# Kernel optimization log

Measured on AMD Instinct MI355X. Metric: run time of the kernel, lower is better.

The kernel has to match this reference:

```python
import jax, jax.numpy as jnp
import numpy as np

N_NODES = 100000
N_EDGES = 3200000
F_IN = 256
N_CLASSES = 10


def setup_inputs() -> dict:
    key = jax.random.key(0)
    ks = jax.random.split(key, 10)
    x = jax.random.normal(ks[0], (N_NODES, F_IN), dtype=jnp.float32)
    edge_index = jax.random.randint(ks[1], (2, N_EDGES), 0, N_NODES, dtype=jnp.int64)
    def glorot(k, fan_in, fan_out):
        s = (6.0 / (fan_in + fan_out)) ** 0.5
        return jax.random.uniform(k, (fan_in, fan_out), jnp.float32, -s, s)
    return {
        "x": x,
        "edge_index": edge_index,
        "W_gcn": glorot(ks[2], F_IN, 64),
        "b_gcn": jnp.zeros((64,), jnp.float32),
        "W1": glorot(ks[3], 64, 32),
        "b1": jnp.zeros((32,), jnp.float32),
        "W2": glorot(ks[4], 32, 16),
        "b2": jnp.zeros((16,), jnp.float32),
        "W3": glorot(ks[5], 16, N_CLASSES),
        "b3": jnp.zeros((N_CLASSES,), jnp.float32),
    }


def gcn_conv(x, edge_index, W, b):
    # PyG GCNConv: x' = D^{-1/2} (A + I) D^{-1/2} (x W) + b, with self-loops.
    n = x.shape[0]
    loop = jnp.arange(n, dtype=edge_index.dtype)
    src = jnp.concatenate([edge_index[0], loop])  # [E+N]
    dst = jnp.concatenate([edge_index[1], loop])
    deg = jax.ops.segment_sum(jnp.ones(src.shape, jnp.float32), dst, num_segments=n)
    dinv = jnp.where(deg > 0, jax.lax.rsqrt(deg), 0.0)
    norm = dinv[src] * dinv[dst]  # [E+N]
    h = x @ W  # transform first (reduces message width to 64)
    msg = h[src] * norm[:, None]  # gather + scale
    out = jax.ops.segment_sum(msg, dst, num_segments=n)  # scatter-add
    return out + b


def reference(x, edge_index, W_gcn, b_gcn, W1, b1, W2, b2, W3, b3):
    # Dropout is a no-op in eval mode; reference uses deterministic eval math.
    h = jax.nn.relu(gcn_conv(x, edge_index, W_gcn, b_gcn))
    h = jax.nn.relu(h @ W1 + b1)
    h = jax.nn.relu(h @ W2 + b2)
    return h @ W3 + b3
```

## Files before the change

### kernel.cpp

```cpp
#include <hip/hip_runtime.h>

#define F_IN 256
#define CHUNK 8192
#define PMAX 24

typedef short bf8_t __attribute__((ext_vector_type(8)));
typedef float f4_t  __attribute__((ext_vector_type(4)));

__device__ __forceinline__ unsigned short f2bf(float f) {
  unsigned u = __float_as_uint(f);
  unsigned r = (u + 0x7FFFu + ((u >> 16) & 1u)) >> 16;
  return (unsigned short)r;
}
#define BF_LO(d) __uint_as_float((d) << 16)
#define BF_HI(d) __uint_as_float((d) & 0xFFFF0000u)

__global__ __launch_bounds__(256) void gemm_mfma_kernel(
    const float* __restrict__ x, const float* __restrict__ W,
    const float* __restrict__ dinvp, unsigned short* __restrict__ hb, int M) {
  __shared__ short As[128][40];
  __shared__ short Bs[64][264];
  const int t = threadIdx.x;
  const int brow = blockIdx.x * 128;
  const int w = t >> 6;
  const int l = t & 63;
  const int mlane = l & 15;
  const int quad = l >> 4;

  for (int i = 0; i < 64; ++i) {
    const int flat = i * 256 + t;
    const int k = flat >> 6, n = flat & 63;
    Bs[n][k] = (short)f2bf(W[flat]);
  }

  f4_t acc[2][4];
#pragma unroll
  for (int a = 0; a < 2; ++a)
#pragma unroll
    for (int b = 0; b < 4; ++b) acc[a][b] = (f4_t){0.f, 0.f, 0.f, 0.f};

  for (int k0 = 0; k0 < F_IN; k0 += 32) {
    {
      const int q = t & 7;
      const int rbase = t >> 3;
#pragma unroll
      for (int j = 0; j < 4; ++j) {
        const int r = rbase + j * 32;
        const int row = brow + r;
        float4 v = make_float4(0.f, 0.f, 0.f, 0.f);
        if (row < M) v = *(const float4*)(x + (size_t)row * F_IN + k0 + (q << 2));
        short* p = &As[r][q << 2];
        p[0] = (short)f2bf(v.x);
        p[1] = (short)f2bf(v.y);
        p[2] = (short)f2bf(v.z);
        p[3] = (short)f2bf(v.w);
      }
    }
    __syncthreads();
    bf8_t afr[2], bfr[4];
#pragma unroll
    for (int mt = 0; mt < 2; ++mt)
      afr[mt] = *(const bf8_t*)&As[w * 32 + mt * 16 + mlane][quad << 3];
#pragma unroll
    for (int nt = 0; nt < 4; ++nt)
      bfr[nt] = *(const bf8_t*)&Bs[nt * 16 + mlane][k0 + (quad << 3)];
#pragma unroll
    for (int mt = 0; mt < 2; ++mt)
#pragma unroll
      for (int nt = 0; nt < 4; ++nt)
        acc[mt][nt] = __builtin_amdgcn_mfma_f32_16x16x32_bf16(
            afr[mt], bfr[nt], acc[mt][nt], 0, 0, 0);
    __syncthreads();
  }

#pragma unroll
  for (int mt = 0; mt < 2; ++mt) {
#pragma unroll
    for (int reg = 0; reg < 4; ++reg) {
      const int row = brow + w * 32 + mt * 16 + (quad << 2) + reg;
      if (row < M) {
        const float di = dinvp[row];
#pragma unroll
        for (int nt = 0; nt < 4; ++nt)
          hb[(size_t)row * 64 + nt * 16 + mlane] = f2bf(di * acc[mt][nt][reg]);
      }
    }
  }
}

__global__ __launch_bounds__(512) void sort_local_kernel(
    const int* __restrict__ src_arr, const int* __restrict__ dst_arr,
    int* __restrict__ espB, int* __restrict__ segStart, int* __restrict__ segCnt,
    int* __restrict__ bucketCount, int E, int NBK) {
  __shared__ int hist[512];
  __shared__ int s[512];
  __shared__ int cur[512];
  const int t = threadIdx.x;
  const int blk = blockIdx.x;
  const int base = blk * CHUNK;
  const int cnt = min(CHUNK, E - base);
  for (int i = t; i < NBK; i += 512) hist[i] = 0;
  __syncthreads();
  int pk[16], bk[16];
#pragma unroll
  for (int k = 0; k < 16; ++k) {
    const int i = t + k * 512;
    bk[k] = -1;
    if (i < cnt) {
      const int sv = src_arr[base + i];
      const int dv = dst_arr[base + i];
      pk[k] = sv | ((dv & 255) << 24);
      bk[k] = dv >> 8;
      atomicAdd(&hist[bk[k]], 1);
    }
  }
  __syncthreads();
  const int v = (t < NBK) ? hist[t] : 0;
  s[t] = v;
  __syncthreads();
#pragma unroll
  for (int off = 1; off < 512; off <<= 1) {
    int add = (t >= off) ? s[t - off] : 0;
    __syncthreads();
    s[t] += add;
    __syncthreads();
  }
  if (t < NBK) {
    const int excl = s[t] - v;
    cur[t] = excl;
    segStart[blk * NBK + t] = base + excl;
    segCnt[blk * NBK + t] = v;
    if (v) atomicAdd(&bucketCount[t], v);
  }
  __syncthreads();
#pragma unroll
  for (int k = 0; k < 16; ++k) {
    if (bk[k] >= 0) {
      const int pos = atomicAdd(&cur[bk[k]], 1);
      espB[base + pos] = pk[k];
    }
  }
}

__global__ __launch_bounds__(512) void scan_buckets_kernel(
    const int* __restrict__ bucketCount, int* __restrict__ bucketStart, int NBK) {
  __shared__ int s[512];
  const int t = threadIdx.x;
  const int v = (t < NBK) ? bucketCount[t] : 0;
  s[t] = v;
  __syncthreads();
#pragma unroll
  for (int off = 1; off < 512; off <<= 1) {
    int add = (t >= off) ? s[t - off] : 0;
    __syncthreads();
    s[t] += add;
    __syncthreads();
  }
  if (t < NBK) bucketStart[t] = s[t] - v;
  if (t == NBK - 1) bucketStart[NBK] = s[t];
}

__global__ __launch_bounds__(512) void fine_bin2_kernel(
    const int* __restrict__ espB, const int* __restrict__ segStart,
    const int* __restrict__ segCnt, const int* __restrict__ bucketStart,
    int* __restrict__ es, int* __restrict__ rowptr, float* __restrict__ dinvp,
    int N, int E, int NBK, int NCH) {
  __shared__ int segO[513];
  __shared__ int segS[512];
  __shared__ int s[512];
  __shared__ int hist[256];
  __shared__ int cur[256];
  const int t = threadIdx.x;
  const int b = blockIdx.x;
  int c = 0;
  if (t < NCH) {
    segS[t] = segStart[t * NBK + b];
    c = segCnt[t * NBK + b];
  }
  s[t] = c;
  if (t < 256) hist[t] = 0;
  __syncthreads();
#pragma unroll
  for (int off = 1; off < 512; off <<= 1) {
    int add = (t >= off) ? s[t - off] : 0;
    __syncthreads();
    s[t] += add;
    __syncthreads();
  }
  segO[t + 1] = s[t];
  if (t == 0) segO[0] = 0;
  __syncthreads();
  const int total = segO[NCH];
  const int base = bucketStart[b];

  int pc[PMAX];
  int it = 0;
  for (int j = t; j < total; j += 512, ++it) {
    int lo = 0, hi = NCH;
    while (hi - lo > 1) {
      const int mid = (lo + hi) >> 1;
      if (segO[mid] <= j) lo = mid; else hi = mid;
    }
    const int p = espB[segS[lo] + (j - segO[lo])];
    if (it < PMAX) pc[it] = p;
    atomicAdd(&hist[((unsigned)p) >> 24], 1);
  }
  __syncthreads();
  const int v2 = (t < 256) ? hist[t] : 0;
  s[t] = v2;
  __syncthreads();
#pragma unroll
  for (int off = 1; off < 256; off <<= 1) {
    int add = (t >= off) ? s[t - off] : 0;
    __syncthreads();
    s[t] += add;
    __syncthreads();
  }
  if (t < 256) {
    const int excl = s[t] - v2;
    cur[t] = base + excl;
    const int node = b * 256 + t;
    if (node < N) {
      rowptr[node] = base + excl;
      dinvp[node] = rsqrtf((float)(v2 + 1));
    }
  }
  if (b == 0 && t == 0) rowptr[N] = E;
  __syncthreads();
  it = 0;
  for (int j = t; j < total; j += 512, ++it) {
    int p;
    if (it < PMAX) {
      p = pc[it];
    } else {
      int lo = 0, hi = NCH;
      while (hi - lo > 1) {
        const int mid = (lo + hi) >> 1;
        if (segO[mid] <= j) lo = mid; else hi = mid;
      }
      p = espB[segS[lo] + (j - segO[lo])];
    }
    const int pos = atomicAdd(&cur[((unsigned)p) >> 24], 1);
    es[pos] = p & 0x00FFFFFF;
  }
}

__global__ __launch_bounds__(256) void agg_csr_kernel(
    const unsigned short* __restrict__ hb, const int* __restrict__ es,
    const int* __restrict__ rowptr, const float* __restrict__ dinvp,
    float* __restrict__ agg, int N) {
  const int t = threadIdx.x;
  const int node = blockIdx.x * 4 + (t >> 6);
  if (node >= N) return;
  const int lane = t & 63;
  const int slot = lane >> 3;
  const int fq = (lane & 7) << 3;
  const int start = rowptr[node];
  const int end = rowptr[node + 1];

  float acc[8] = {0.f};
  int i = start + slot;
  for (; i + 8 < end; i += 16) {
    const int s0 = es[i];
    const int s1 = es[i + 8];
    const uint4 r0 = *(const uint4*)(hb + (size_t)s0 * 64 + fq);
    const uint4 r1 = *(const uint4*)(hb + (size_t)s1 * 64 + fq);
    acc[0] += BF_LO(r0.x) + BF_LO(r1.x);
    acc[1] += BF_HI(r0.x) + BF_HI(r1.x);
    acc[2] += BF_LO(r0.y) + BF_LO(r1.y);
    acc[3] += BF_HI(r0.y) + BF_HI(r1.y);
    acc[4] += BF_LO(r0.z) + BF_LO(r1.z);
    acc[5] += BF_HI(r0.z) + BF_HI(r1.z);
    acc[6] += BF_LO(r0.w) + BF_LO(r1.w);
    acc[7] += BF_HI(r0.w) + BF_HI(r1.w);
  }
  if (i < end) {
    const int s0 = es[i];
    const uint4 r0 = *(const uint4*)(hb + (size_t)s0 * 64 + fq);
    acc[0] += BF_LO(r0.x);
    acc[1] += BF_HI(r0.x);
    acc[2] += BF_LO(r0.y);
    acc[3] += BF_HI(r0.y);
    acc[4] += BF_LO(r0.z);
    acc[5] += BF_HI(r0.z);
    acc[6] += BF_LO(r0.w);
    acc[7] += BF_HI(r0.w);
  }
#pragma unroll
  for (int m = 8; m <= 32; m <<= 1)
#pragma unroll
    for (int j = 0; j < 8; ++j) acc[j] += __shfl_xor(acc[j], m, 64);

  if (slot == 0) {
    const float di = dinvp[node];
    float4 o0 = make_float4(acc[0] * di, acc[1] * di, acc[2] * di, acc[3] * di);
    float4 o1 = make_float4(acc[4] * di, acc[5] * di, acc[6] * di, acc[7] * di);
    float* ap = agg + (size_t)node * 64 + fq;
    *(float4*)(ap + 0) = o0;
    *(float4*)(ap + 4) = o1;
  }
}

__global__ __launch_bounds__(256) void mlp_kernel(
    const float* __restrict__ agg, const unsigned short* __restrict__ hb,
    const float* __restrict__ dinvp, const float* __restrict__ bg,
    const float* __restrict__ W1, const float* __restrict__ b1,
    const float* __restrict__ W2, const float* __restrict__ b2,
    const float* __restrict__ W3, const float* __restrict__ b3,
    float* __restrict__ out, int N) {
  __shared__ float W1T[32][64];
  __shared__ float W2T[16][32];
  __shared__ float W3T[10][16];
  __shared__ float b1s[32], b2s[16], b3s[10], bgs[64];
  const int t = threadIdx.x;
  for (int i = t; i < 2048; i += 256) W1T[i >> 6][i & 63] = W1[(i & 63) * 32 + (i >> 6)];
  for (int i = t; i < 512; i += 256)  W2T[i >> 5][i & 31] = W2[(i & 31) * 16 + (i >> 5)];
  for (int i = t; i < 160; i += 256)  W3T[i >> 4][i & 15] = W3[(i & 15) * 10 + (i >> 4)];
  if (t < 64) bgs[t] = bg[t];
  if (t < 32) b1s[t] = b1[t];
  if (t < 16) b2s[t] = b2[t];
  if (t < 10) b3s[t] = b3[t];
  __syncthreads();

  const int node = blockIdx.x * 256 + t;
  if (node >= N) return;
  const float di = dinvp[node];

  float g[64];
#pragma unroll
  for (int k = 0; k < 64; k += 8) {
    const float4 a0 = *(const float4*)(agg + (size_t)node * 64 + k);
    const float4 a1 = *(const float4*)(agg + (size_t)node * 64 + k + 4);
    const uint4 r = *(const uint4*)(hb + (size_t)node * 64 + k);
    g[k + 0] = fmaxf(a0.x + di * BF_LO(r.x) + bgs[k + 0], 0.f);
    g[k + 1] = fmaxf(a0.y + di * BF_HI(r.x) + bgs[k + 1], 0.f);
    g[k + 2] = fmaxf(a0.z + di * BF_LO(r.y) + bgs[k + 2], 0.f);
    g[k + 3] = fmaxf(a0.w + di * BF_HI(r.y) + bgs[k + 3], 0.f);
    g[k + 4] = fmaxf(a1.x + di * BF_LO(r.z) + bgs[k + 4], 0.f);
    g[k + 5] = fmaxf(a1.y + di * BF_HI(r.z) + bgs[k + 5], 0.f);
    g[k + 6] = fmaxf(a1.z + di * BF_LO(r.w) + bgs[k + 6], 0.f);
    g[k + 7] = fmaxf(a1.w + di * BF_HI(r.w) + bgs[k + 7], 0.f);
  }

  float h1[32];
#pragma unroll
  for (int j = 0; j < 32; ++j) {
    float acc = b1s[j];
#pragma unroll
    for (int k = 0; k < 64; k += 4) {
      const float4 w = *(const float4*)&W1T[j][k];
      acc += g[k] * w.x + g[k + 1] * w.y + g[k + 2] * w.z + g[k + 3] * w.w;
    }
    h1[j] = fmaxf(acc, 0.f);
  }

  float h2[16];
#pragma unroll
  for (int j = 0; j < 16; ++j) {
    float acc = b2s[j];
#pragma unroll
    for (int k = 0; k < 32; k += 4) {
      const float4 w = *(const float4*)&W2T[j][k];
      acc += h1[k] * w.x + h1[k + 1] * w.y + h1[k + 2] * w.z + h1[k + 3] * w.w;
    }
    h2[j] = fmaxf(acc, 0.f);
  }

#pragma unroll
  for (int j = 0; j < 10; ++j) {
    float acc = b3s[j];
#pragma unroll
    for (int k = 0; k < 16; k += 4) {
      const float4 w = *(const float4*)&W3T[j][k];
      acc += h2[k] * w.x + h2[k + 1] * w.y + h2[k + 2] * w.z + h2[k + 3] * w.w;
    }
    out[(size_t)node * 10 + j] = acc;
  }
}

extern "C" void kernel_launch(void* const* d_in, const int* in_sizes, int n_in,
                              void* d_out, int out_size, void* d_ws, size_t ws_size,
                              hipStream_t stream) {
  const float* x     = (const float*)d_in[0];
  const int*   ei    = (const int*)d_in[1];
  const float* W_gcn = (const float*)d_in[2];
  const float* b_gcn = (const float*)d_in[3];
  const float* W1    = (const float*)d_in[4];
  const float* b1    = (const float*)d_in[5];
  const float* W2    = (const float*)d_in[6];
  const float* b2    = (const float*)d_in[7];
  const float* W3    = (const float*)d_in[8];
  const float* b3    = (const float*)d_in[9];
  float* out = (float*)d_out;

  const int N = in_sizes[0] / F_IN;
  const int E = in_sizes[1] / 2;
  const int* src = ei;
  const int* dst = ei + E;
  const int NBK = (N + 255) >> 8;
  const int NCH = (E + CHUNK - 1) / CHUNK;

  unsigned short* hb = (unsigned short*)d_ws;
  float* dinvp       = (float*)(hb + (size_t)N * 64);
  int*   es          = (int*)(dinvp + N);
  int*   rowptr      = es + E;
  int*   bucketCount = rowptr + N + 16;
  int*   bucketStart = bucketCount + 512;
  int*   espB        = bucketStart + 528;
  int*   segStart    = espB + E;
  int*   segCnt      = segStart + NCH * NBK;
  float* agg         = (float*)espB;

  hipMemsetAsync(bucketCount, 0, 512 * sizeof(int), stream);

  sort_local_kernel<<<NCH, 512, 0, stream>>>(
      src, dst, espB, segStart, segCnt, bucketCount, E, NBK);
  scan_buckets_kernel<<<1, 512, 0, stream>>>(bucketCount, bucketStart, NBK);
  fine_bin2_kernel<<<NBK, 512, 0, stream>>>(
      espB, segStart, segCnt, bucketStart, es, rowptr, dinvp, N, E, NBK, NCH);

  gemm_mfma_kernel<<<(N + 127) / 128, 256, 0, stream>>>(x, W_gcn, dinvp, hb, N);

  agg_csr_kernel<<<(N + 3) / 4, 256, 0, stream>>>(hb, es, rowptr, dinvp, agg, N);

  mlp_kernel<<<(N + 255) / 256, 256, 0, stream>>>(
      agg, hb, dinvp, b_gcn, W1, b1, W2, b2, W3, b3, out, N);
}
```

Baseline: 367.9 us.

## Use MFMA bf16 for MLP head and simplify fine binning traversal

The per-node scalar FP32 MLP (64→32→16→10) is replaced by a block-tiled version that stages activations and weights in shared memory as bf16 and computes each layer with 16x16x32 bf16 MFMA instructions. The fine binning kernel drops its prefix scan over segments and the per-element binary search, and instead has each wavefront walk segments directly for both the histogram and scatter passes. This trades FP32 precision in the MLP for matrix-core throughput, and it removes register caching of edge values, so espB is read twice.

```diff
diff --git a/kernel.cpp b/kernel.cpp
--- a/kernel.cpp
+++ b/kernel.cpp
@@ -2,7 +2,6 @@
 
 #define F_IN 256
 #define CHUNK 8192
-#define PMAX 24
 
 typedef short bf8_t __attribute__((ext_vector_type(8)));
 typedef float f4_t  __attribute__((ext_vector_type(4)));
@@ -165,59 +164,46 @@
     const int* __restrict__ segCnt, const int* __restrict__ bucketStart,
     int* __restrict__ es, int* __restrict__ rowptr, float* __restrict__ dinvp,
     int N, int E, int NBK, int NCH) {
-  __shared__ int segO[513];
   __shared__ int segS[512];
-  __shared__ int s[512];
+  __shared__ int segC[512];
+  __shared__ int sbuf[512];
   __shared__ int hist[256];
   __shared__ int cur[256];
   const int t = threadIdx.x;
   const int b = blockIdx.x;
-  int c = 0;
-  if (t < NCH) {
-    segS[t] = segStart[t * NBK + b];
-    c = segCnt[t * NBK + b];
-  }
-  s[t] = c;
+  for (int i = t; i < 512; i += 512) { segS[i] = 0; segC[i] = 0; }
   if (t < 256) hist[t] = 0;
   __syncthreads();
-#pragma unroll
-  for (int off = 1; off < 512; off <<= 1) {
-    int add = (t >= off) ? s[t - off] : 0;
-    __syncthreads();
-    s[t] += add;
-    __syncthreads();
-  }
-  segO[t + 1] = s[t];
-  if (t == 0) segO[0] = 0;
-  __syncthreads();
-  const int total = segO[NCH];
+  for (int i = t; i < NCH; i += 512) {
+    segS[i] = segStart[i * NBK + b];
+    segC[i] = segCnt[i * NBK + b];
+  }
+  __syncthreads();
+
+  const int wid = t >> 6;
+  const int lane = t & 63;
+
+  for (int seg = wid; seg < NCH; seg += 8) {
+    const int sS = segS[seg], c = segC[seg];
+    for (int j = lane; j < c; j += 64)
+      atomicAdd(&hist[((unsigned)espB[sS + j]) >> 24], 1);
+  }
+  __syncthreads();
+
+  int v2 = 0;
+  if (t < 256) { v2 = hist[t]; sbuf[t] = v2; }
+  __syncthreads();
+#pragma unroll
+  for (int off = 1; off < 256; off <<= 1) {
+    int add = 0;
+    if (t < 256 && t >= off) add = sbuf[t - off];
+    __syncthreads();
+    if (t < 256) sbuf[t] += add;
+    __syncthreads();
+  }
   const int base = bucketStart[b];
-
-  int pc[PMAX];
-  int it = 0;
-  for (int j = t; j < total; j += 512, ++it) {
-    int lo = 0, hi = NCH;
-    while (hi - lo > 1) {
-      const int mid = (lo + hi) >> 1;
-      if (segO[mid] <= j) lo = mid; else hi = mid;
-    }
-    const int p = espB[segS[lo] + (j - segO[lo])];
-    if (it < PMAX) pc[it] = p;
-    atomicAdd(&hist[((unsigned)p) >> 24], 1);
-  }
-  __syncthreads();
-  const int v2 = (t < 256) ? hist[t] : 0;
-  s[t] = v2;
-  __syncthreads();
-#pragma unroll
-  for (int off = 1; off < 256; off <<= 1) {
-    int add = (t >= off) ? s[t - off] : 0;
-    __syncthreads();
-    s[t] += add;
-    __syncthreads();
-  }
   if (t < 256) {
-    const int excl = s[t] - v2;
+    const int excl = sbuf[t] - v2;
     cur[t] = base + excl;
     const int node = b * 256 + t;
     if (node < N) {
@@ -227,21 +213,14 @@
   }
   if (b == 0 && t == 0) rowptr[N] = E;
   __syncthreads();
-  it = 0;
-  for (int j = t; j < total; j += 512, ++it) {
-    int p;
-    if (it < PMAX) {
-      p = pc[it];
-    } else {
-      int lo = 0, hi = NCH;
-      while (hi - lo > 1) {
-        const int mid = (lo + hi) >> 1;
-        if (segO[mid] <= j) lo = mid; else hi = mid;
-      }
-      p = espB[segS[lo] + (j - segO[lo])];
-    }
-    const int pos = atomicAdd(&cur[((unsigned)p) >> 24], 1);
-    es[pos] = p & 0x00FFFFFF;
+
+  for (int seg = wid; seg < NCH; seg += 8) {
+    const int sS = segS[seg], c = segC[seg];
+    for (int j = lane; j < c; j += 64) {
+      const int p = espB[sS + j];
+      const int pos = atomicAdd(&cur[((unsigned)p) >> 24], 1);
+      es[pos] = p & 0x00FFFFFF;
+    }
   }
 }
 
@@ -301,80 +280,132 @@
   }
 }
 
-__global__ __launch_bounds__(256) void mlp_kernel(
+__global__ __launch_bounds__(256) void mlp_mfma_kernel(
     const float* __restrict__ agg, const unsigned short* __restrict__ hb,
     const float* __restrict__ dinvp, const float* __restrict__ bg,
     const float* __restrict__ W1, const float* __restrict__ b1,
     const float* __restrict__ W2, const float* __restrict__ b2,
     const float* __restrict__ W3, const float* __restrict__ b3,
     float* __restrict__ out, int N) {
-  __shared__ float W1T[32][64];
-  __shared__ float W2T[16][32];
-  __shared__ float W3T[10][16];
-  __shared__ float b1s[32], b2s[16], b3s[10], bgs[64];
-  const int t = threadIdx.x;
-  for (int i = t; i < 2048; i += 256) W1T[i >> 6][i & 63] = W1[(i & 63) * 32 + (i >> 6)];
-  for (int i = t; i < 512; i += 256)  W2T[i >> 5][i & 31] = W2[(i & 31) * 16 + (i >> 5)];
-  for (int i = t; i < 160; i += 256)  W3T[i >> 4][i & 15] = W3[(i & 15) * 10 + (i >> 4)];
+  __shared__ short g64[256 * 72];
+  __shared__ short h2s[256 * 40];
+  __shared__ short W1s[32 * 72];
+  __shared__ short W2s[16 * 40];
+  __shared__ short W3s[16 * 40];
+  __shared__ float bgs[64], b1s[32], b2s[16], b3s[16];
+  short* h1s = g64;
+
+  const int t = threadIdx.x;
+  const int node0 = blockIdx.x * 256;
+  for (int i = t; i < 256 * 40; i += 256) h2s[i] = 0;
+  for (int i = t; i < 16 * 40; i += 256) W3s[i] = 0;
   if (t < 64) bgs[t] = bg[t];
   if (t < 32) b1s[t] = b1[t];
-  if (t < 16) b2s[t] = b2[t];
-  if (t < 10) b3s[t] = b3[t];
-  __syncthreads();
-
-  const int node = blockIdx.x * 256 + t;
-  if (node >= N) return;
-  const float di = dinvp[node];
-
-  float g[64];
-#pragma unroll
-  for (int k = 0; k < 64; k += 8) {
-    const float4 a0 = *(const float4*)(agg + (size_t)node * 64 + k);
-    const float4 a1 = *(const float4*)(agg + (size_t)node * 64 + k + 4);
-    const uint4 r = *(const uint4*)(hb + (size_t)node * 64 + k);
-    g[k + 0] = fmaxf(a0.x + di * BF_LO(r.x) + bgs[k + 0], 0.f);
-    g[k + 1] = fmaxf(a0.y + di * BF_HI(r.x) + bgs[k + 1], 0.f);
-    g[k + 2] = fmaxf(a0.z + di * BF_LO(r.y) + bgs[k + 2], 0.f);
-    g[k + 3] = fmaxf(a0.w + di * BF_HI(r.y) + bgs[k + 3], 0.f);
-    g[k + 4] = fmaxf(a1.x + di * BF_LO(r.z) + bgs[k + 4], 0.f);
-    g[k + 5] = fmaxf(a1.y + di * BF_HI(r.z) + bgs[k + 5], 0.f);
-    g[k + 6] = fmaxf(a1.z + di * BF_LO(r.w) + bgs[k + 6], 0.f);
-    g[k + 7] = fmaxf(a1.w + di * BF_HI(r.w) + bgs[k + 7], 0.f);
-  }
-
-  float h1[32];
-#pragma unroll
-  for (int j = 0; j < 32; ++j) {
-    float acc = b1s[j];
-#pragma unroll
-    for (int k = 0; k < 64; k += 4) {
-      const float4 w = *(const float4*)&W1T[j][k];
-      acc += g[k] * w.x + g[k + 1] * w.y + g[k + 2] * w.z + g[k + 3] * w.w;
-    }
-    h1[j] = fmaxf(acc, 0.f);
-  }
-
-  float h2[16];
-#pragma unroll
-  for (int j = 0; j < 16; ++j) {
-    float acc = b2s[j];
-#pragma unroll
-    for (int k = 0; k < 32; k += 4) {
-      const float4 w = *(const float4*)&W2T[j][k];
-      acc += h1[k] * w.x + h1[k + 1] * w.y + h1[k + 2] * w.z + h1[k + 3] * w.w;
-    }
-    h2[j] = fmaxf(acc, 0.f);
-  }
-
-#pragma unroll
-  for (int j = 0; j < 10; ++j) {
-    float acc = b3s[j];
-#pragma unroll
-    for (int k = 0; k < 16; k += 4) {
-      const float4 w = *(const float4*)&W3T[j][k];
-      acc += h2[k] * w.x + h2[k + 1] * w.y + h2[k + 2] * w.z + h2[k + 3] * w.w;
-    }
-    out[(size_t)node * 10 + j] = acc;
+  if (t < 16) { b2s[t] = b2[t]; b3s[t] = (t < 10) ? b3[t] : 0.f; }
+  __syncthreads();
+  for (int i = t; i < 2048; i += 256) { const int k = i >> 5, n = i & 31; W1s[n * 72 + k] = (short)f2bf(W1[i]); }
+  for (int i = t; i < 512;  i += 256) { const int k = i >> 4, n = i & 15; W2s[n * 40 + k] = (short)f2bf(W2[i]); }
+  if (t < 160) { const int k = t / 10, n = t % 10; W3s[n * 40 + k] = (short)f2bf(W3[t]); }
+  {
+    const int nd = min(node0 + t, N - 1);
+    const float di = dinvp[nd];
+    short* gr = &g64[t * 72];
+    const float* ar = agg + (size_t)nd * 64;
+    const unsigned short* hr = hb + (size_t)nd * 64;
+#pragma unroll
+    for (int k = 0; k < 64; k += 8) {
+      const float4 a0 = *(const float4*)(ar + k);
+      const float4 a1 = *(const float4*)(ar + k + 4);
+      const uint4 r = *(const uint4*)(hr + k);
+      gr[k + 0] = (short)f2bf(fmaxf(a0.x + di * BF_LO(r.x) + bgs[k + 0], 0.f));
+      gr[k + 1] = (short)f2bf(fmaxf(a0.y + di * BF_HI(r.x) + bgs[k + 1], 0.f));
+      gr[k + 2] = (short)f2bf(fmaxf(a0.z + di * BF_LO(r.y) + bgs[k + 2], 0.f));
+      gr[k + 3] = (short)f2bf(fmaxf(a0.w + di * BF_HI(r.y) + bgs[k + 3], 0.f));
+      gr[k + 4] = (short)f2bf(fmaxf(a1.x + di * BF_LO(r.z) + bgs[k + 4], 0.f));
+      gr[k + 5] = (short)f2bf(fmaxf(a1.y + di * BF_HI(r.z) + bgs[k + 5], 0.f));
+      gr[k + 6] = (short)f2bf(fmaxf(a1.z + di * BF_LO(r.w) + bgs[k + 6], 0.f));
+      gr[k + 7] = (short)f2bf(fmaxf(a1.w + di * BF_HI(r.w) + bgs[k + 7], 0.f));
+    }
+  }
+  __syncthreads();
+
+  const int w = t >> 6;
+  const int lane = t & 63;
+  const int ml = lane & 15;
+  const int quad = lane >> 4;
+
+  bf8_t a1f[4][2], b1f[2][2];
+#pragma unroll
+  for (int mt = 0; mt < 4; ++mt)
+#pragma unroll
+    for (int ks = 0; ks < 2; ++ks)
+      a1f[mt][ks] = *(const bf8_t*)&g64[(w * 64 + mt * 16 + ml) * 72 + ks * 32 + quad * 8];
+#pragma unroll
+  for (int nt = 0; nt < 2; ++nt)
+#pragma unroll
+    for (int ks = 0; ks < 2; ++ks)
+      b1f[nt][ks] = *(const bf8_t*)&W1s[(nt * 16 + ml) * 72 + ks * 32 + quad * 8];
+  f4_t acc1[4][2];
+#pragma unroll
+  for (int mt = 0; mt < 4; ++mt)
+#pragma unroll
+    for (int nt = 0; nt < 2; ++nt) acc1[mt][nt] = (f4_t){0.f, 0.f, 0.f, 0.f};
+#pragma unroll
+  for (int ks = 0; ks < 2; ++ks)
+#pragma unroll
+    for (int mt = 0; mt < 4; ++mt)
+#pragma unroll
+      for (int nt = 0; nt < 2; ++nt)
+        acc1[mt][nt] = __builtin_amdgcn_mfma_f32_16x16x32_bf16(
+            a1f[mt][ks], b1f[nt][ks], acc1[mt][nt], 0, 0, 0);
+  __syncthreads();
+#pragma unroll
+  for (int mt = 0; mt < 4; ++mt)
+#pragma unroll
+    for (int nt = 0; nt < 2; ++nt)
+#pragma unroll
+      for (int reg = 0; reg < 4; ++reg) {
+        const int row = w * 64 + mt * 16 + quad * 4 + reg;
+        const int col = nt * 16 + ml;
+        h1s[row * 40 + col] = (short)f2bf(fmaxf(acc1[mt][nt][reg] + b1s[col], 0.f));
+      }
+  __syncthreads();
+
+  bf8_t a2f[4];
+#pragma unroll
+  for (int mt = 0; mt < 4; ++mt)
+    a2f[mt] = *(const bf8_t*)&h1s[(w * 64 + mt * 16 + ml) * 40 + quad * 8];
+  const bf8_t b2f = *(const bf8_t*)&W2s[ml * 40 + quad * 8];
+  f4_t acc2[4];
+#pragma unroll
+  for (int mt = 0; mt < 4; ++mt) {
+    acc2[mt] = (f4_t){0.f, 0.f, 0.f, 0.f};
+    acc2[mt] = __builtin_amdgcn_mfma_f32_16x16x32_bf16(a2f[mt], b2f, acc2[mt], 0, 0, 0);
+  }
+  __syncthreads();
+#pragma unroll
+  for (int mt = 0; mt < 4; ++mt)
+#pragma unroll
+    for (int reg = 0; reg < 4; ++reg) {
+      const int row = w * 64 + mt * 16 + quad * 4 + reg;
+      h2s[row * 40 + ml] = (short)f2bf(fmaxf(acc2[mt][reg] + b2s[ml], 0.f));
+    }
+  __syncthreads();
+
+  bf8_t a3f[4];
+#pragma unroll
+  for (int mt = 0; mt < 4; ++mt)
+    a3f[mt] = *(const bf8_t*)&h2s[(w * 64 + mt * 16 + ml) * 40 + quad * 8];
+  const bf8_t b3f = *(const bf8_t*)&W3s[ml * 40 + quad * 8];
+#pragma unroll
+  for (int mt = 0; mt < 4; ++mt) {
+    f4_t acc3 = (f4_t){0.f, 0.f, 0.f, 0.f};
+    acc3 = __builtin_amdgcn_mfma_f32_16x16x32_bf16(a3f[mt], b3f, acc3, 0, 0, 0);
+#pragma unroll
+    for (int reg = 0; reg < 4; ++reg) {
+      const int node = node0 + w * 64 + mt * 16 + quad * 4 + reg;
+      if (ml < 10 && node < N) out[(size_t)node * 10 + ml] = acc3[reg] + b3s[ml];
+    }
   }
 }
 
@@ -423,6 +454,6 @@
 
   agg_csr_kernel<<<(N + 3) / 4, 256, 0, stream>>>(hb, es, rowptr, dinvp, agg, N);
 
-  mlp_kernel<<<(N + 255) / 256, 256, 0, stream>>>(
+  mlp_mfma_kernel<<<(N + 255) / 256, 256, 0, stream>>>(
       agg, hb, dinvp, b_gcn, W1, b1, W2, b2, W3, b3, out, N);
 }
```

New measurement: 360.4 us. -2.0%, faster.
